# Optimization experiments

Hardware: AMD Instinct MI355X
Metric: run time of the kernel (lower is better)

The kernel has to match this reference:

```python
import jax, jax.numpy as jnp
import numpy as np

D = 256      # model dim
H = 8        # heads
DK = D // H  # head dim = 32
HID = 4 * D  # mlp hidden = 1024
B, S = 8, 1024
NUM_REL = 10  # rel-pos embedding vocab, padding_idx = 9


def _ln(x, g, b):
    m = jnp.mean(x, axis=-1, keepdims=True)
    v = jnp.var(x, axis=-1, keepdims=True)
    return (x - m) * jax.lax.rsqrt(v + 1e-5) * g + b


def setup_inputs() -> dict:
    key = jax.random.key(0)
    ks = jax.random.split(key, 16)
    s = 0.02
    x = jax.random.normal(ks[0], (B, S, D), jnp.float32)
    rel_pos = jax.random.randint(ks[1], (B, S, S), 0, NUM_REL, jnp.int64)
    adj = jax.random.uniform(ks[2], (B, S, S), jnp.float32)
    # attention params (Linear weights stored as [in, out])
    Wk = jax.random.normal(ks[3], (D, D), jnp.float32) * s
    Wv = jax.random.normal(ks[4], (D, D), jnp.float32) * s
    Wq = jax.random.normal(ks[5], (D, D), jnp.float32) * s
    Wo = jax.random.normal(ks[6], (D, D), jnp.float32) * s
    bk = jnp.zeros((D,)); bv = jnp.zeros((D,)); bq = jnp.zeros((D,)); bo = jnp.zeros((D,))
    # rel-pos embedding tables [10, H], padding row 9 zeroed (padding_idx=9)
    emb_f = (jax.random.normal(ks[7], (NUM_REL, H), jnp.float32) * s).at[NUM_REL - 1].set(0.0)
    emb_b = (jax.random.normal(ks[8], (NUM_REL, H), jnp.float32) * s).at[NUM_REL - 1].set(0.0)
    # GCN-MLP params
    W1 = jax.random.normal(ks[9], (D, HID), jnp.float32) * s
    Wg = jax.random.normal(ks[10], (D, HID), jnp.float32) * s
    W2 = jax.random.normal(ks[11], (HID, D), jnp.float32) * s
    b1 = jnp.zeros((HID,)); bg = jnp.zeros((HID,)); b2 = jnp.zeros((D,))
    return {
        "x": x, "rel_pos": rel_pos, "adj": adj,
        "ln1_g": jnp.ones((D,)), "ln1_b": jnp.zeros((D,)),
        "Wk": Wk, "bk": bk, "Wv": Wv, "bv": bv, "Wq": Wq, "bq": bq,
        "Wo": Wo, "bo": bo, "emb_f": emb_f, "emb_b": emb_b,
        "ln2_g": jnp.ones((D,)), "ln2_b": jnp.zeros((D,)),
        "W1": W1, "b1": b1, "Wg": Wg, "bg": bg, "W2": W2, "b2": b2,
    }


def reference(x, rel_pos, adj, ln1_g, ln1_b, Wk, bk, Wv, bv, Wq, bq, Wo, bo,
              emb_f, emb_b, ln2_g, ln2_b, W1, b1, Wg, bg, W2, b2):
    b_, s_, _ = x.shape
    # --- self-attention block (pre-LN, residual) ---
    xn = _ln(x, ln1_g, ln1_b)
    q = (xn @ Wq + bq).reshape(b_, s_, H, DK).transpose(0, 2, 1, 3)  # [B,H,S,dk]
    k = (xn @ Wk + bk).reshape(b_, s_, H, DK).transpose(0, 2, 1, 3)
    v = (xn @ Wv + bv).reshape(b_, s_, H, DK).transpose(0, 2, 1, 3)
    # multiplicative relative-position bias: [B,S,S,H] -> [B,H,S,S]
    bias = emb_f[rel_pos] + emb_b[jnp.swapaxes(rel_pos, -2, -1)]
    bias = jnp.transpose(bias, (0, 3, 1, 2))
    scores = jnp.einsum('bhqd,bhkd->bhqk', q, k) / np.sqrt(DK).astype(np.float32)
    scores = scores * (1.0 + bias)
    p = jax.nn.softmax(scores, axis=-1)
    o = jnp.einsum('bhqk,bhkd->bhqd', p, v).transpose(0, 2, 1, 3).reshape(b_, s_, D)
    x = x + (o @ Wo + bo)
    # --- GCN feed-forward block (pre-LN, residual) ---
    xn = _ln(x, ln2_g, ln2_b)
    x1 = xn @ W1 + b1                       # [B,S,HID]
    g = xn @ Wg + bg                        # [B,S,HID]
    g1, g2 = jnp.split(g, 2, axis=-1)       # each [B,S,HID/2]
    h = x1 + jnp.concatenate([
        jnp.einsum('bij,bjd->bid', adj, g1),      # adj @ g1
        jnp.einsum('bji,bjd->bid', adj, g2),      # adj.mT @ g2
    ], axis=-1)
    h = jax.nn.relu(h)
    return x + (h @ W2 + b2)
```

## Files before the change

### kernel.cpp

```cpp
#include <hip/hip_runtime.h>
#include <hip/hip_bf16.h>

#define SS 1024
#define DD 256
#define HH 8
#define DKK 32
#define HIDD 1024
#define BB 8

typedef unsigned short ushort_t;
typedef __attribute__((ext_vector_type(8))) short bf16x8;
typedef __attribute__((ext_vector_type(4))) float f32x4;
typedef __attribute__((ext_vector_type(16))) float f32x16;

__device__ __forceinline__ ushort_t f2b(float f) {
    unsigned x = __float_as_uint(f);
    unsigned r = (x + 0x7fffu + ((x >> 16) & 1u)) >> 16;
    return (ushort_t)r;
}
__device__ __forceinline__ float b2f(ushort_t u) {
    return __uint_as_float(((unsigned)u) << 16);
}
__device__ __forceinline__ void gload16(const void* g, void* l) {
    __builtin_amdgcn_global_load_lds(
        (const __attribute__((address_space(1))) unsigned int*)g,
        (__attribute__((address_space(3))) unsigned int*)l, 16, 0, 0);
}

__global__ __launch_bounds__(256) void ln_kernel(const float* __restrict__ in,
    const float* __restrict__ gamma, const float* __restrict__ beta,
    ushort_t* __restrict__ out)
{
    const int row = blockIdx.x;
    const int t = threadIdx.x;
    const float v = in[(long)row * DD + t];
    float s = v, s2 = v * v;
#pragma unroll
    for (int off = 1; off < 64; off <<= 1) {
        s += __shfl_xor(s, off);
        s2 += __shfl_xor(s2, off);
    }
    __shared__ float w1[4], w2[4];
    if ((t & 63) == 0) { w1[t >> 6] = s; w2[t >> 6] = s2; }
    __syncthreads();
    s = w1[0] + w1[1] + w1[2] + w1[3];
    s2 = w2[0] + w2[1] + w2[2] + w2[3];
    const float mean = s * (1.f / DD);
    const float var = s2 * (1.f / DD) - mean * mean;
    const float rs = rsqrtf(var + 1e-5f);
    out[(long)row * DD + t] = f2b((v - mean) * rs * gamma[t] + beta[t]);
}

__global__ __launch_bounds__(256) void wtrans_all(
    const float* __restrict__ Wq, const float* __restrict__ Wk,
    const float* __restrict__ Wv, const float* __restrict__ Wo,
    const float* __restrict__ W1, const float* __restrict__ Wg,
    const float* __restrict__ W2,
    ushort_t* __restrict__ WqkvT, ushort_t* __restrict__ WoT,
    ushort_t* __restrict__ W1gT, ushort_t* __restrict__ W2T,
    const float* __restrict__ bq, const float* __restrict__ bk,
    const float* __restrict__ bv, const float* __restrict__ b1,
    const float* __restrict__ bg, float* __restrict__ bqkv, float* __restrict__ b1g)
{
    int t = blockIdx.x;
    const int tid = threadIdx.x;
    if (blockIdx.x == 0) {
        for (int i = tid; i < 768; i += 256)
            bqkv[i] = (i < 256) ? bq[i] : ((i < 512) ? bk[i - 256] : bv[i - 512]);
        for (int i = tid; i < 2048; i += 256)
            b1g[i] = (i < 1024) ? b1[i] : bg[i - 1024];
    }
    const float* src; ushort_t* dst; int R, C;
    if (t < 64)        { src = Wq; dst = WqkvT;              R = DD;   C = DD; }
    else if (t < 128)  { src = Wk; dst = WqkvT + 256 * 256;  R = DD;   C = DD;   t -= 64; }
    else if (t < 192)  { src = Wv; dst = WqkvT + 512 * 256;  R = DD;   C = DD;   t -= 128; }
    else if (t < 256)  { src = Wo; dst = WoT;                R = DD;   C = DD;   t -= 192; }
    else if (t < 512)  { src = W1; dst = W1gT;               R = DD;   C = HIDD; t -= 256; }
    else if (t < 768)  { src = Wg; dst = W1gT + 1024 * 256;  R = DD;   C = HIDD; t -= 512; }
    else               { src = W2; dst = W2T;                R = HIDD; C = DD;   t -= 768; }
    const int tilesC = C >> 5;
    const int r0 = (t / tilesC) * 32, c0 = (t % tilesC) * 32;
    __shared__ float tt[32][33];
    const int i = tid >> 3, j0 = (tid & 7) << 2;
    const float4 v = *(const float4*)(src + (long)(r0 + i) * C + c0 + j0);
    tt[i][j0 + 0] = v.x; tt[i][j0 + 1] = v.y; tt[i][j0 + 2] = v.z; tt[i][j0 + 3] = v.w;
    __syncthreads();
    ushort4 o;
    o.x = f2b(tt[j0 + 0][i]); o.y = f2b(tt[j0 + 1][i]);
    o.z = f2b(tt[j0 + 2][i]); o.w = f2b(tt[j0 + 3][i]);
    *(ushort4*)(dst + (long)(c0 + i) * R + r0 + j0) = o;
}

__global__ __launch_bounds__(256) void adjconv(const float* __restrict__ adj,
    ushort_t* __restrict__ adjb, ushort_t* __restrict__ adjTb)
{
    const int c0 = blockIdx.x * 32, r0 = blockIdx.y * 32;
    const long base = (long)blockIdx.z * SS * SS;
    __shared__ float t[32][33];
    const int tid = threadIdx.x;
    const int i = tid >> 3, j0 = (tid & 7) << 2;
    const float4 v = *(const float4*)(adj + base + (long)(r0 + i) * SS + c0 + j0);
    t[i][j0 + 0] = v.x; t[i][j0 + 1] = v.y; t[i][j0 + 2] = v.z; t[i][j0 + 3] = v.w;
    ushort4 oc;
    oc.x = f2b(v.x); oc.y = f2b(v.y); oc.z = f2b(v.z); oc.w = f2b(v.w);
    *(ushort4*)(adjb + base + (long)(r0 + i) * SS + c0 + j0) = oc;
    __syncthreads();
    ushort4 ot;
    ot.x = f2b(t[j0 + 0][i]); ot.y = f2b(t[j0 + 1][i]);
    ot.z = f2b(t[j0 + 2][i]); ot.w = f2b(t[j0 + 3][i]);
    *(ushort4*)(adjTb + base + (long)(c0 + i) * SS + r0 + j0) = ot;
}

__global__ __launch_bounds__(256) void pack_kernel(const int* __restrict__ rp,
    unsigned char* __restrict__ packed)
{
    const int kt = blockIdx.x, qt = blockIdx.y, b = blockIdx.z;
    __shared__ int tA[32][33];
    __shared__ int tB[32][33];
    const int tid = threadIdx.x;
    const int i = tid >> 3;
    const int j0 = (tid & 7) << 2;
    const long base = (long)b * SS * SS;
    const int4 a4 = *(const int4*)(rp + base + (long)(qt * 32 + i) * SS + kt * 32 + j0);
    tA[i][j0 + 0] = a4.x; tA[i][j0 + 1] = a4.y; tA[i][j0 + 2] = a4.z; tA[i][j0 + 3] = a4.w;
    const int4 b4 = *(const int4*)(rp + base + (long)(kt * 32 + i) * SS + qt * 32 + j0);
    tB[i][j0 + 0] = b4.x; tB[i][j0 + 1] = b4.y; tB[i][j0 + 2] = b4.z; tB[i][j0 + 3] = b4.w;
    __syncthreads();
    uchar4 o4;
    o4.x = (unsigned char)(tA[i][j0 + 0] + 10 * tB[j0 + 0][i]);
    o4.y = (unsigned char)(tA[i][j0 + 1] + 10 * tB[j0 + 1][i]);
    o4.z = (unsigned char)(tA[i][j0 + 2] + 10 * tB[j0 + 2][i]);
    o4.w = (unsigned char)(tA[i][j0 + 3] + 10 * tB[j0 + 3][i]);
    *(uchar4*)(packed + base + (long)(qt * 32 + i) * SS + kt * 32 + j0) = o4;
}

template<int MODE, bool RELU, int BN, bool SPLITZ>
__global__ __launch_bounds__(256) void mgemm(
    const ushort_t* __restrict__ A, const ushort_t* __restrict__ BT,
    const float* __restrict__ bias, const void* __restrict__ Res,
    void* __restrict__ C, void* __restrict__ C2,
    int M, int N, int K, int lda, int ldbt, int ldc,
    long sA, long sBT, long sC, long sRes, long tbStride, int tbRows, int nsplit)
{
    const int z = blockIdx.z;
    long coff;
    const ushort_t* Ap; const ushort_t* Bp;
    if (SPLITZ) {
        const int zb = z & 7, hf = z >> 3;
        Ap = A + (long)z * sA;
        Bp = BT + (long)zb * sBT + (long)hf * tbStride;
        coff = (long)zb * sC + (long)hf * nsplit;
    } else {
        Ap = A + (long)z * sA;
        Bp = BT + (long)z * sBT;
        coff = (long)z * sC;
    }
    const int n0 = blockIdx.x * BN, m0 = blockIdx.y * 128;
    const int tid = threadIdx.x, wid = tid >> 6, lane = tid & 63;
    const int wr = wid >> 1, wc = wid & 1;
    const int l4 = lane & 15, lh = lane >> 4;
    constexpr int NF = BN / 32;
    __shared__ ushort_t Asb[128 * 64];
    __shared__ ushort_t Bsb[BN * 64];
    const int srow = lane >> 3;
    const int scol = 8 * ((lane & 7) ^ srow);
    f32x4 acc[4][NF] = {};
    for (int k0 = 0; k0 < K; k0 += 64) {
#pragma unroll
        for (int i = 0; i < 4; i++) {
            const int l = wid * 4 + i;
            gload16(Ap + (long)(m0 + l * 8 + srow) * lda + k0 + scol, &Asb[l * 512]);
        }
#pragma unroll
        for (int i = 0; i < NF; i++) {
            const int l = wid * NF + i;
            gload16(Bp + (long)(n0 + l * 8 + srow) * ldbt + k0 + scol, &Bsb[l * 512]);
        }
        __syncthreads();
        bf16x8 af[2][4], bfr[2][NF];
#pragma unroll
        for (int mi = 0; mi < 4; mi++) {
            const int row = wr * 64 + mi * 16 + l4;
            const int sw = (row & 7) << 3;
            af[0][mi] = *(const bf16x8*)&Asb[row * 64 + ((lh * 8) ^ sw)];
            af[1][mi] = *(const bf16x8*)&Asb[row * 64 + ((32 + lh * 8) ^ sw)];
        }
#pragma unroll
        for (int nj = 0; nj < NF; nj++) {
            const int row = wc * (BN / 2) + nj * 16 + l4;
            const int sw = (row & 7) << 3;
            bfr[0][nj] = *(const bf16x8*)&Bsb[row * 64 + ((lh * 8) ^ sw)];
            bfr[1][nj] = *(const bf16x8*)&Bsb[row * 64 + ((32 + lh * 8) ^ sw)];
        }
        __builtin_amdgcn_s_setprio(1);
#pragma unroll
        for (int kk = 0; kk < 2; kk++)
#pragma unroll
            for (int mi = 0; mi < 4; mi++)
#pragma unroll
                for (int nj = 0; nj < NF; nj++)
                    acc[mi][nj] = __builtin_amdgcn_mfma_f32_16x16x32_bf16(
                        af[kk][mi], bfr[kk][nj], acc[mi][nj], 0, 0, 0);
        __builtin_amdgcn_s_setprio(0);
        __syncthreads();
    }
#pragma unroll
    for (int mi = 0; mi < 4; mi++) {
#pragma unroll
        for (int nj = 0; nj < NF; nj++) {
            const int n = n0 + wc * (BN / 2) + nj * 16 + l4;
            const int mb = m0 + wr * 64 + mi * 16 + lh * 4;
            const float bv = bias ? bias[n] : 0.f;
            if (MODE == 0) {
                float* Cp = (float*)C + coff;
                const float* Rp = Res ? (const float*)Res + (long)z * sRes : (const float*)0;
#pragma unroll
                for (int r = 0; r < 4; r++) {
                    float v = acc[mi][nj][r] + bv;
                    if (Rp) v += Rp[(long)(mb + r) * ldc + n];
                    if (RELU) v = fmaxf(v, 0.f);
                    Cp[(long)(mb + r) * ldc + n] = v;
                }
            } else if (MODE == 1) {
                ushort_t* Cp = (ushort_t*)C + coff;
                const ushort_t* Rp = Res ? (const ushort_t*)Res + coff : (const ushort_t*)0;
#pragma unroll
                for (int r = 0; r < 4; r++) {
                    float v = acc[mi][nj][r] + bv;
                    if (Rp) v += b2f(Rp[(long)(mb + r) * ldc + n]);
                    if (RELU) v = fmaxf(v, 0.f);
                    Cp[(long)(mb + r) * ldc + n] = f2b(v);
                }
            } else {
                const int nb = n0 + wc * (BN / 2) + nj * 16;
                if (nb < nsplit) {
                    ushort_t* Cp = (ushort_t*)C;
#pragma unroll
                    for (int r = 0; r < 4; r++)
                        Cp[(long)(mb + r) * ldc + n] = f2b(acc[mi][nj][r] + bv);
                } else {
                    ushort_t* Cp = (ushort_t*)C2;
                    const int bidx = mb / tbRows;
                    const int s = mb - bidx * tbRows;
                    ushort4 o4;
                    o4.x = f2b(acc[mi][nj][0] + bv);
                    o4.y = f2b(acc[mi][nj][1] + bv);
                    o4.z = f2b(acc[mi][nj][2] + bv);
                    o4.w = f2b(acc[mi][nj][3] + bv);
                    *(ushort4*)(Cp + (long)bidx * tbStride + (long)(n - nsplit) * tbRows + s) = o4;
                }
            }
        }
    }
}

__global__ __launch_bounds__(256) void attn3(
    const ushort_t* __restrict__ qk, const ushort_t* __restrict__ vt,
    const unsigned char* __restrict__ pkd,
    const float* __restrict__ ef, const float* __restrict__ eb,
    ushort_t* __restrict__ ob)
{
    const int h = blockIdx.y, b = blockIdx.z;
    const int tid = threadIdx.x;
    const int wid = tid >> 6, lane = tid & 63;
    const int l31 = lane & 31, hi = lane >> 5;
    __shared__ float tm[100];
    __shared__ float cacc[3][64][20];
    __shared__ float cl[3][64];
    if (tid < 100)
        tm[tid] = 0.25506953899092946f
                  * (1.f + ef[(tid % 10) * HH + h] + eb[(tid / 10) * HH + h]);
    __syncthreads();
    const int q0 = blockIdx.x * 32;
    const ushort_t* qrow = qk + ((long)(b * SS + q0 + l31)) * 512 + h * DKK + hi * 8;
    const bf16x8 qlo = *(const bf16x8*)(qrow);
    const bf16x8 qhi = *(const bf16x8*)(qrow + 16);
    const unsigned char* prow = pkd + ((long)(b * SS + q0 + l31)) * SS;
    const ushort_t* vrow = vt + ((long)(b * DD + h * DKK + l31)) * SS + hi * 8;
    const ushort_t* krow = qk + ((long)(b * SS + l31)) * 512 + 256 + h * DKK + hi * 8;
    f32x16 acc = {};
    float lrun = 0.f;
    const int kbase = wid * 256;
#pragma unroll 2
    for (int it = 0; it < 8; it++) {
        const int kt = kbase + it * 32;
        const ushort_t* kp = krow + (long)kt * 512;
        const bf16x8 klo = *(const bf16x8*)kp;
        const bf16x8 khi = *(const bf16x8*)(kp + 16);
        f32x16 sf = {};
        __builtin_amdgcn_s_setprio(1);
        sf = __builtin_amdgcn_mfma_f32_32x32x16_bf16(klo, qlo, sf, 0, 0, 0);
        sf = __builtin_amdgcn_mfma_f32_32x32x16_bf16(khi, qhi, sf, 0, 0, 0);
        __builtin_amdgcn_s_setprio(0);
        const uint4 u0 = *(const uint4*)(prow + kt);
        const uint4 u1 = *(const uint4*)(prow + kt + 16);
        const unsigned wa = hi ? u0.y : u0.x;
        const unsigned wb = hi ? u0.w : u0.z;
        const unsigned wc2 = hi ? u1.y : u1.x;
        const unsigned wd = hi ? u1.w : u1.z;
        float p[16];
#pragma unroll
        for (int rb = 0; rb < 4; rb++) {
            p[0 + rb]  = __builtin_amdgcn_exp2f(sf[0 + rb]  * tm[(wa  >> (8 * rb)) & 255u]);
            p[4 + rb]  = __builtin_amdgcn_exp2f(sf[4 + rb]  * tm[(wb  >> (8 * rb)) & 255u]);
            p[8 + rb]  = __builtin_amdgcn_exp2f(sf[8 + rb]  * tm[(wc2 >> (8 * rb)) & 255u]);
            p[12 + rb] = __builtin_amdgcn_exp2f(sf[12 + rb] * tm[(wd  >> (8 * rb)) & 255u]);
        }
        float ts = 0.f;
#pragma unroll
        for (int r = 0; r < 16; r++) ts += p[r];
        lrun += ts + __shfl_xor(ts, 32);
        unsigned cw[8];
#pragma unroll
        for (int i = 0; i < 8; i++)
            asm("v_cvt_pk_bf16_f32 %0, %1, %2" : "=v"(cw[i]) : "v"(p[2 * i]), "v"(p[2 * i + 1]));
        unsigned dw[8];
#pragma unroll
        for (int i = 0; i < 8; i++) dw[i] = (unsigned)__shfl_xor((int)cw[i], 32);
        union { unsigned u[8]; bf16x8 v[2]; } fu;
        fu.u[0] = hi ? dw[2] : cw[0]; fu.u[1] = hi ? dw[3] : cw[1];
        fu.u[2] = hi ? cw[2] : dw[0]; fu.u[3] = hi ? cw[3] : dw[1];
        fu.u[4] = hi ? dw[6] : cw[4]; fu.u[5] = hi ? dw[7] : cw[5];
        fu.u[6] = hi ? cw[6] : dw[4]; fu.u[7] = hi ? cw[7] : dw[5];
        const bf16x8 vlo = *(const bf16x8*)(vrow + kt);
        const bf16x8 vhi = *(const bf16x8*)(vrow + kt + 16);
        __builtin_amdgcn_s_setprio(1);
        acc = __builtin_amdgcn_mfma_f32_32x32x16_bf16(vlo, fu.v[0], acc, 0, 0, 0);
        acc = __builtin_amdgcn_mfma_f32_32x32x16_bf16(vhi, fu.v[1], acc, 0, 0, 0);
        __builtin_amdgcn_s_setprio(0);
    }
    if (wid != 0) {
        float* cp = &cacc[wid - 1][lane][0];
#pragma unroll
        for (int r = 0; r < 16; r++) cp[r] = acc[r];
        cl[wid - 1][lane] = lrun;
    }
    __syncthreads();
    if (wid == 0) {
#pragma unroll
        for (int w = 0; w < 3; w++) {
            const float* cp = &cacc[w][lane][0];
#pragma unroll
            for (int r = 0; r < 16; r++) acc[r] += cp[r];
            lrun += cl[w][lane];
        }
        const float invl = 1.f / lrun;
        ushort_t* orow = ob + ((long)(b * SS + q0 + l31)) * DD + h * DKK + 4 * hi;
#pragma unroll
        for (int g = 0; g < 4; g++) {
            ushort4 o4;
            o4.x = f2b(acc[4 * g + 0] * invl);
            o4.y = f2b(acc[4 * g + 1] * invl);
            o4.z = f2b(acc[4 * g + 2] * invl);
            o4.w = f2b(acc[4 * g + 3] * invl);
            *(ushort4*)(orow + 8 * g) = o4;
        }
    }
}

extern "C" void kernel_launch(void* const* d_in, const int* in_sizes, int n_in,
                              void* d_out, int out_size, void* d_ws, size_t ws_size,
                              hipStream_t stream)
{
    const float* x    = (const float*)d_in[0];
    const int*   rp   = (const int*)d_in[1];
    const float* adj  = (const float*)d_in[2];
    const float* ln1g = (const float*)d_in[3];
    const float* ln1b = (const float*)d_in[4];
    const float* Wk   = (const float*)d_in[5];
    const float* bk   = (const float*)d_in[6];
    const float* Wv   = (const float*)d_in[7];
    const float* bv   = (const float*)d_in[8];
    const float* Wq   = (const float*)d_in[9];
    const float* bq   = (const float*)d_in[10];
    const float* Wo   = (const float*)d_in[11];
    const float* bo   = (const float*)d_in[12];
    const float* embf = (const float*)d_in[13];
    const float* embb = (const float*)d_in[14];
    const float* ln2g = (const float*)d_in[15];
    const float* ln2b = (const float*)d_in[16];
    const float* W1   = (const float*)d_in[17];
    const float* b1   = (const float*)d_in[18];
    const float* Wg   = (const float*)d_in[19];
    const float* bg   = (const float*)d_in[20];
    const float* W2   = (const float*)d_in[21];
    const float* b2   = (const float*)d_in[22];
    float* out = (float*)d_out;

    char* ws = (char*)d_ws;
    const long MB = 1ll << 20;
    ushort_t* qkb = (ushort_t*)(ws + 0);
    ushort_t* vtb = (ushort_t*)(ws + 8 * MB);
    ushort_t* obb = (ushort_t*)(ws + 12 * MB);
    unsigned char* pkb = (unsigned char*)(ws + 16 * MB);
    ushort_t* xnb = (ushort_t*)(ws + 24 * MB);
    ushort_t* x1hb = (ushort_t*)(ws + 0);
    ushort_t* gtb  = (ushort_t*)(ws + 16 * MB);
    ushort_t* adjb  = (ushort_t*)(ws + 32 * MB);
    ushort_t* adjTb = (ushort_t*)(ws + 48 * MB);
    float*    x2    = (float*)(ws + 64 * MB);
    ushort_t* xn2b  = (ushort_t*)(ws + 72 * MB);
    ushort_t* wT    = (ushort_t*)(ws + 76 * MB);
    ushort_t* WqkvT = wT;
    ushort_t* WoT   = wT + 768 * 256;
    ushort_t* W1gT  = wT + 768 * 256 + 256 * 256;
    ushort_t* W2T   = W1gT + 2048 * 256;
    float* bqkv = (float*)(ws + 78 * MB);
    float* b1g  = bqkv + 768;

    const int rows = BB * SS;
    dim3 blk(256);

    wtrans_all<<<1024, blk, 0, stream>>>(Wq, Wk, Wv, Wo, W1, Wg, W2,
                                         WqkvT, WoT, W1gT, W2T,
                                         bq, bk, bv, b1, bg, bqkv, b1g);
    ln_kernel<<<rows, blk, 0, stream>>>(x, ln1g, ln1b, xnb);
    mgemm<3, false, 64, false><<<dim3(12, 64, 1), blk, 0, stream>>>(
        xnb, WqkvT, bqkv, nullptr, qkb, vtb, rows, 768, DD, DD, DD, 512,
        0, 0, 0, 0, (long)DD * SS, SS, 512);
    pack_kernel<<<dim3(32, 32, 8), blk, 0, stream>>>(rp, pkb);
    adjconv<<<dim3(32, 32, 8), blk, 0, stream>>>(adj, adjb, adjTb);
    attn3<<<dim3(32, 8, 8), blk, 0, stream>>>(qkb, vtb, pkb, embf, embb, obb);
    mgemm<0, false, 64, false><<<dim3(4, 64, 1), blk, 0, stream>>>(
        obb, WoT, bo, x, x2, nullptr, rows, DD, DD, DD, DD, DD,
        0, 0, 0, 0, 0, 1, 0);
    ln_kernel<<<rows, blk, 0, stream>>>(x2, ln2g, ln2b, xn2b);
    mgemm<3, false, 128, false><<<dim3(16, 64, 1), blk, 0, stream>>>(
        xn2b, W1gT, b1g, nullptr, x1hb, gtb, rows, 2048, DD, DD, DD, HIDD,
        0, 0, 0, 0, (long)HIDD * SS, SS, 1024);
    mgemm<1, true, 64, true><<<dim3(8, 8, 16), blk, 0, stream>>>(
        adjb, gtb, nullptr, x1hb, x1hb, nullptr, SS, 512, SS, SS, SS, HIDD,
        (long)SS * SS, (long)HIDD * SS, (long)SS * HIDD, 0, (long)512 * SS, SS, 512);
    mgemm<0, false, 64, false><<<dim3(4, 64, 1), blk, 0, stream>>>(
        x1hb, W2T, b2, x2, out, nullptr, rows, DD, HIDD, HIDD, HIDD, DD,
        0, 0, 0, 0, 0, 1, 0);
}
```

Baseline: 357.5 us.

## Keep residual stream in bf16 and remap block grids for XCD locality

The first LayerNorm now also writes a bf16 copy of x. The attention output projection writes a bf16 residual x2, which the second LayerNorm and the final GEMM (new MODE 4, bf16 residual to fp32 output) read. This cuts fp32 residual traffic but rounds the residual stream to bf16, which risks accuracy. The attention and adjacency GEMM launches are flattened to 1D grids with a swizzle that groups blocks of the same batch/head onto the same XCD, and the adjacency GEMM tile width BN is raised from 64 to 128.

```diff
diff --git a/kernel.cpp b/kernel.cpp
--- a/kernel.cpp
+++ b/kernel.cpp
@@ -27,13 +27,16 @@
         (__attribute__((address_space(3))) unsigned int*)l, 16, 0, 0);
 }
 
-__global__ __launch_bounds__(256) void ln_kernel(const float* __restrict__ in,
+template<bool INBF, bool EMIT>
+__global__ __launch_bounds__(256) void ln_kernel(const void* __restrict__ in,
     const float* __restrict__ gamma, const float* __restrict__ beta,
-    ushort_t* __restrict__ out)
+    ushort_t* __restrict__ out, ushort_t* __restrict__ raw)
 {
     const int row = blockIdx.x;
     const int t = threadIdx.x;
-    const float v = in[(long)row * DD + t];
+    float v;
+    if (INBF) v = b2f(((const ushort_t*)in)[(long)row * DD + t]);
+    else      v = ((const float*)in)[(long)row * DD + t];
     float s = v, s2 = v * v;
 #pragma unroll
     for (int off = 1; off < 64; off <<= 1) {
@@ -48,6 +51,7 @@
     const float mean = s * (1.f / DD);
     const float var = s2 * (1.f / DD) - mean * mean;
     const float rs = rsqrtf(var + 1e-5f);
+    if (EMIT) raw[(long)row * DD + t] = f2b(v);
     out[(long)row * DD + t] = f2b((v - mean) * rs * gamma[t] + beta[t]);
 }
 
@@ -142,7 +146,17 @@
     int M, int N, int K, int lda, int ldbt, int ldc,
     long sA, long sBT, long sC, long sRes, long tbStride, int tbRows, int nsplit)
 {
-    const int z = blockIdx.z;
+    int n0, m0, z;
+    if (SPLITZ) {
+        const int fid = blockIdx.x;
+        const int glin = ((fid & 7) << 6) + (fid >> 3);
+        z = glin >> 5;
+        const int xy = glin & 31;
+        n0 = (xy & 3) * BN;
+        m0 = (xy >> 2) * 128;
+    } else {
+        n0 = blockIdx.x * BN; m0 = blockIdx.y * 128; z = blockIdx.z;
+    }
     long coff;
     const ushort_t* Ap; const ushort_t* Bp;
     if (SPLITZ) {
@@ -155,7 +169,6 @@
         Bp = BT + (long)z * sBT;
         coff = (long)z * sC;
     }
-    const int n0 = blockIdx.x * BN, m0 = blockIdx.y * 128;
     const int tid = threadIdx.x, wid = tid >> 6, lane = tid & 63;
     const int wr = wid >> 1, wc = wid & 1;
     const int l4 = lane & 15, lh = lane >> 4;
@@ -211,17 +224,7 @@
             const int n = n0 + wc * (BN / 2) + nj * 16 + l4;
             const int mb = m0 + wr * 64 + mi * 16 + lh * 4;
             const float bv = bias ? bias[n] : 0.f;
-            if (MODE == 0) {
-                float* Cp = (float*)C + coff;
-                const float* Rp = Res ? (const float*)Res + (long)z * sRes : (const float*)0;
-#pragma unroll
-                for (int r = 0; r < 4; r++) {
-                    float v = acc[mi][nj][r] + bv;
-                    if (Rp) v += Rp[(long)(mb + r) * ldc + n];
-                    if (RELU) v = fmaxf(v, 0.f);
-                    Cp[(long)(mb + r) * ldc + n] = v;
-                }
-            } else if (MODE == 1) {
+            if (MODE == 1) {
                 ushort_t* Cp = (ushort_t*)C + coff;
                 const ushort_t* Rp = Res ? (const ushort_t*)Res + coff : (const ushort_t*)0;
 #pragma unroll
@@ -230,6 +233,15 @@
                     if (Rp) v += b2f(Rp[(long)(mb + r) * ldc + n]);
                     if (RELU) v = fmaxf(v, 0.f);
                     Cp[(long)(mb + r) * ldc + n] = f2b(v);
+                }
+            } else if (MODE == 4) {
+                float* Cp = (float*)C;
+                const ushort_t* Rp = (const ushort_t*)Res;
+#pragma unroll
+                for (int r = 0; r < 4; r++) {
+                    float v = acc[mi][nj][r] + bv + b2f(Rp[(long)(mb + r) * ldc + n]);
+                    if (RELU) v = fmaxf(v, 0.f);
+                    Cp[(long)(mb + r) * ldc + n] = v;
                 }
             } else {
                 const int nb = n0 + wc * (BN / 2) + nj * 16;
@@ -260,7 +272,11 @@
     const float* __restrict__ ef, const float* __restrict__ eb,
     ushort_t* __restrict__ ob)
 {
-    const int h = blockIdx.y, b = blockIdx.z;
+    const int fid = blockIdx.x;
+    const int glin = ((fid & 7) << 8) + (fid >> 3);
+    const int bh = glin >> 5;
+    const int qt = glin & 31;
+    const int b = bh >> 3, h = bh & 7;
     const int tid = threadIdx.x;
     const int wid = tid >> 6, lane = tid & 63;
     const int l31 = lane & 31, hi = lane >> 5;
@@ -271,7 +287,7 @@
         tm[tid] = 0.25506953899092946f
                   * (1.f + ef[(tid % 10) * HH + h] + eb[(tid / 10) * HH + h]);
     __syncthreads();
-    const int q0 = blockIdx.x * 32;
+    const int q0 = qt * 32;
     const ushort_t* qrow = qk + ((long)(b * SS + q0 + l31)) * 512 + h * DKK + hi * 8;
     const bf16x8 qlo = *(const bf16x8*)(qrow);
     const bf16x8 qhi = *(const bf16x8*)(qrow + 16);
@@ -394,18 +410,19 @@
     ushort_t* obb = (ushort_t*)(ws + 12 * MB);
     unsigned char* pkb = (unsigned char*)(ws + 16 * MB);
     ushort_t* xnb = (ushort_t*)(ws + 24 * MB);
+    ushort_t* xb  = (ushort_t*)(ws + 28 * MB);
     ushort_t* x1hb = (ushort_t*)(ws + 0);
     ushort_t* gtb  = (ushort_t*)(ws + 16 * MB);
-    ushort_t* adjb  = (ushort_t*)(ws + 32 * MB);
-    ushort_t* adjTb = (ushort_t*)(ws + 48 * MB);
-    float*    x2    = (float*)(ws + 64 * MB);
-    ushort_t* xn2b  = (ushort_t*)(ws + 72 * MB);
-    ushort_t* wT    = (ushort_t*)(ws + 76 * MB);
+    ushort_t* x2b  = (ushort_t*)(ws + 32 * MB);
+    ushort_t* xn2b = (ushort_t*)(ws + 36 * MB);
+    ushort_t* adjb  = (ushort_t*)(ws + 40 * MB);
+    ushort_t* adjTb = (ushort_t*)(ws + 56 * MB);
+    ushort_t* wT    = (ushort_t*)(ws + 72 * MB);
     ushort_t* WqkvT = wT;
     ushort_t* WoT   = wT + 768 * 256;
     ushort_t* W1gT  = wT + 768 * 256 + 256 * 256;
     ushort_t* W2T   = W1gT + 2048 * 256;
-    float* bqkv = (float*)(ws + 78 * MB);
+    float* bqkv = (float*)(ws + 75 * MB);
     float* b1g  = bqkv + 768;
 
     const int rows = BB * SS;
@@ -414,24 +431,24 @@
     wtrans_all<<<1024, blk, 0, stream>>>(Wq, Wk, Wv, Wo, W1, Wg, W2,
                                          WqkvT, WoT, W1gT, W2T,
                                          bq, bk, bv, b1, bg, bqkv, b1g);
-    ln_kernel<<<rows, blk, 0, stream>>>(x, ln1g, ln1b, xnb);
+    ln_kernel<false, true><<<rows, blk, 0, stream>>>(x, ln1g, ln1b, xnb, xb);
     mgemm<3, false, 64, false><<<dim3(12, 64, 1), blk, 0, stream>>>(
         xnb, WqkvT, bqkv, nullptr, qkb, vtb, rows, 768, DD, DD, DD, 512,
         0, 0, 0, 0, (long)DD * SS, SS, 512);
     pack_kernel<<<dim3(32, 32, 8), blk, 0, stream>>>(rp, pkb);
     adjconv<<<dim3(32, 32, 8), blk, 0, stream>>>(adj, adjb, adjTb);
-    attn3<<<dim3(32, 8, 8), blk, 0, stream>>>(qkb, vtb, pkb, embf, embb, obb);
-    mgemm<0, false, 64, false><<<dim3(4, 64, 1), blk, 0, stream>>>(
-        obb, WoT, bo, x, x2, nullptr, rows, DD, DD, DD, DD, DD,
+    attn3<<<dim3(2048, 1, 1), blk, 0, stream>>>(qkb, vtb, pkb, embf, embb, obb);
+    mgemm<1, false, 64, false><<<dim3(4, 64, 1), blk, 0, stream>>>(
+        obb, WoT, bo, xb, x2b, nullptr, rows, DD, DD, DD, DD, DD,
         0, 0, 0, 0, 0, 1, 0);
-    ln_kernel<<<rows, blk, 0, stream>>>(x2, ln2g, ln2b, xn2b);
+    ln_kernel<true, false><<<rows, blk, 0, stream>>>(x2b, ln2g, ln2b, xn2b, nullptr);
     mgemm<3, false, 128, false><<<dim3(16, 64, 1), blk, 0, stream>>>(
         xn2b, W1gT, b1g, nullptr, x1hb, gtb, rows, 2048, DD, DD, DD, HIDD,
         0, 0, 0, 0, (long)HIDD * SS, SS, 1024);
-    mgemm<1, true, 64, true><<<dim3(8, 8, 16), blk, 0, stream>>>(
+    mgemm<1, true, 128, true><<<dim3(512, 1, 1), blk, 0, stream>>>(
         adjb, gtb, nullptr, x1hb, x1hb, nullptr, SS, 512, SS, SS, SS, HIDD,
         (long)SS * SS, (long)HIDD * SS, (long)SS * HIDD, 0, (long)512 * SS, SS, 512);
-    mgemm<0, false, 64, false><<<dim3(4, 64, 1), blk, 0, stream>>>(
-        x1hb, W2T, b2, x2, out, nullptr, rows, DD, HIDD, HIDD, HIDD, DD,
+    mgemm<4, false, 64, false><<<dim3(4, 64, 1), blk, 0, stream>>>(
+        x1hb, W2T, b2, x2b, out, nullptr, rows, DD, HIDD, HIDD, HIDD, DD,
         0, 0, 0, 0, 0, 1, 0);
 }
```

New measurement: 337.5 us. -5.6%, faster.
